# Kernel optimization log

Hardware: AMD Instinct MI355X
Metric: run time of the kernel (lower is better)

Reference implementation:

```python
import jax, jax.numpy as jnp
import numpy as np

B, L, D = 4, 2048, 2048
NH, HD, K = 32, 64, 16
LR = 1.0
EPS = 1e-6


def ln_fwd(x, gamma, beta):
    mu = x.mean(-1, keepdims=True)
    var = jnp.var(x, axis=-1, keepdims=True)
    x_hat = (x - mu) / jnp.sqrt(var + EPS)
    return gamma * x_hat + beta


def ln_fused_l2_bwd(x, target, gamma, beta):
    # grad of 0.5*||LN(x)-target||^2 wrt x (matches LayerNormFunction.backward
    # with grad_output = LN(x) - target)
    d = x.shape[-1]
    mu = x.mean(-1, keepdims=True)
    var = jnp.var(x, axis=-1, keepdims=True)
    std = jnp.sqrt(var + EPS)
    x_hat = (x - mu) / std
    y = gamma * x_hat + beta
    g = (y - target) * gamma
    return (d * g - g.sum(-1, keepdims=True) - x_hat * (g * x_hat).sum(-1, keepdims=True)) / (d * std)


def setup_inputs() -> dict:
    key = jax.random.key(0)
    ks = jax.random.split(key, 12)
    s = 0.02
    return {
        "hidden_states": jax.random.normal(ks[0], (B, L, D), jnp.float32),
        "Wq": jax.random.normal(ks[1], (D, D), jnp.float32) * s,
        "Wk": jax.random.normal(ks[2], (D, D), jnp.float32) * s,
        "Wv": jax.random.normal(ks[3], (D, D), jnp.float32) * s,
        "Wo": jax.random.normal(ks[4], (D, D), jnp.float32) * s,
        "linear_weight": jax.random.normal(ks[5], (NH, 1, D), jnp.float32) * s,
        "linear_bias": jnp.zeros((NH, 1), jnp.float32),
        "ln_weight": jnp.ones((NH, HD), jnp.float32),
        "ln_bias": jnp.zeros((NH, HD), jnp.float32),
        "W1_init": jax.random.normal(ks[6], (NH, HD, HD), jnp.float32) * s,
        "b1_init": jnp.zeros((NH, 1, HD), jnp.float32),
    }


def reference(hidden_states, Wq, Wk, Wv, Wo, linear_weight, linear_bias,
              ln_weight, ln_bias, W1_init, b1_init):
    Bq, Lq, Dq = hidden_states.shape
    n_chunk = Lq // K

    def split(x):  # [B,L,D] -> [B,NH,n_chunk,K,HD]
        return x.reshape(Bq, n_chunk, K, NH, HD).transpose(0, 3, 1, 2, 4)

    XC = split(hidden_states @ Wq.T)
    XB = split(hidden_states @ Wk.T)
    XA = split(hidden_states @ Wv.T)

    # inner-loop learning-rate coefficient: [B,NH,n_chunk,K,1]
    X = hidden_states.reshape(Bq, n_chunk, K, Dq)
    ilr = jnp.einsum('bnkd,hd->bhnk', X, linear_weight[:, 0, :]) + linear_bias[:, 0][None, :, None, None]
    ilr_gated = jax.nn.sigmoid(ilr)[..., None]
    token_idx = 1.0 / jnp.arange(1, K + 1, dtype=hidden_states.dtype)
    coeff = (LR * token_idx).reshape(1, 1, 1, K, 1) * ilr_gated / HD

    ln_w = ln_weight.reshape(1, NH, 1, HD)
    ln_b = ln_bias.reshape(1, NH, 1, HD)
    mask = jnp.tril(jnp.ones((K, K), hidden_states.dtype))

    W1 = jnp.broadcast_to(W1_init[None], (Bq, NH, HD, HD))
    b1 = jnp.broadcast_to(b1_init[None], (Bq, NH, 1, HD))

    def step(carry, inp):
        W1, b1 = carry
        xc, xb, xa, co = inp  # [B,NH,K,HD], co: [B,NH,K,1]
        Z1 = xb @ W1 + b1
        grad = ln_fused_l2_bwd(Z1, xa - xb, ln_w, ln_b)  # [B,NH,K,HD]
        Attn = mask * jnp.einsum('bhkf,bhjf->bhkj', xc, xb)
        E = mask * co.transpose(0, 1, 3, 2)  # E[i,j] = coeff_j * (j<=i)
        b1_bar = b1 - E @ grad
        Z1_bar = xc @ W1 - (Attn * E) @ grad + b1_bar
        W1_new = W1 - jnp.einsum('bhkf,bhkg->bhfg', co * xb, grad)
        b1_new = b1 - (co * grad).sum(-2, keepdims=True)
        out = xc + ln_fwd(Z1_bar, ln_w, ln_b)
        return (W1_new, b1_new), out

    xs = (XC.transpose(2, 0, 1, 3, 4), XB.transpose(2, 0, 1, 3, 4),
          XA.transpose(2, 0, 1, 3, 4), coeff.transpose(2, 0, 1, 3, 4))
    (_, _), outs = jax.lax.scan(step, (W1, b1), xs)
    # outs: [n_chunk,B,NH,K,HD] -> [B,L,D]
    XCW = outs.transpose(1, 0, 3, 2, 4).reshape(Bq, Lq, Dq)
    return XCW @ Wo.T
```

## Files before the change

kernel.cpp:

```cpp
#include <hip/hip_runtime.h>


typedef __attribute__((ext_vector_type(4))) float float4v;
typedef __attribute__((ext_vector_type(8))) __bf16 bf16x8;
typedef __attribute__((ext_vector_type(4))) short short4v;
typedef __attribute__((ext_vector_type(4))) unsigned int uint4v;

__device__ __forceinline__ unsigned short f2bf(float f) {
  unsigned int u = __builtin_bit_cast(unsigned int, f);
  u += 0x7FFFu + ((u >> 16) & 1u);
  return (unsigned short)(u >> 16);
}
__device__ __forceinline__ float bf2f(unsigned short s) {
  unsigned int u = ((unsigned int)s) << 16;
  return __builtin_bit_cast(float, u);
}
__device__ __forceinline__ void lds_load16(const void* g, void* l) {
  __builtin_amdgcn_global_load_lds((const __attribute__((address_space(1))) void*)g,
                                   (__attribute__((address_space(3))) void*)l, 16, 0, 0);
}

__device__ __forceinline__ void store_out(float* p, float v) { *p = v; }
__device__ __forceinline__ void store_out(unsigned short* p, float v) { *p = f2bf(v); }

template <typename OUT>
__global__ __launch_bounds__(256) void gemm_bt(
    const unsigned short* __restrict__ A, const unsigned short* __restrict__ B,
    OUT* __restrict__ C, int M, int N, int K) {
  __shared__ unsigned short sA[128 * 32];
  __shared__ unsigned short sB[128 * 32];
  const int tid = threadIdx.x;
  const int wave = tid >> 6;
  const int lane = tid & 63;
  const int quad = lane >> 4;
  const int l15 = lane & 15;
  const int wm = (wave >> 1) * 64;
  const int wn = (wave & 1) * 64;
  const int bm = blockIdx.y * 128;
  const int bn = blockIdx.x * 128;

  float4v acc[4][4];
#pragma unroll
  for (int i = 0; i < 4; ++i)
#pragma unroll
    for (int j = 0; j < 4; ++j) acc[i][j] = (float4v){0.f, 0.f, 0.f, 0.f};

  const int srow = tid >> 2;
  const int scol = (tid & 3) * 8;
  const unsigned short* aptr = A + (size_t)(bm + srow) * K + scol;
  const unsigned short* bptr = B + (size_t)(bn + srow) * K + scol;
  unsigned short* sAw0 = &sA[wave * 512];
  unsigned short* sAw1 = &sA[2048 + wave * 512];
  unsigned short* sBw0 = &sB[wave * 512];
  unsigned short* sBw1 = &sB[2048 + wave * 512];
  const size_t astep = (size_t)64 * K;

  for (int kt = 0; kt < K; kt += 32) {
    __syncthreads();
    lds_load16(aptr + kt, sAw0);
    lds_load16(aptr + kt + astep, sAw1);
    lds_load16(bptr + kt, sBw0);
    lds_load16(bptr + kt + astep, sBw1);
    __syncthreads();
    bf16x8 af[4], bf[4];
#pragma unroll
    for (int i = 0; i < 4; ++i)
      af[i] = *(const bf16x8*)&sA[(wm + i * 16 + l15) * 32 + quad * 8];
#pragma unroll
    for (int j = 0; j < 4; ++j)
      bf[j] = *(const bf16x8*)&sB[(wn + j * 16 + l15) * 32 + quad * 8];
#pragma unroll
    for (int i = 0; i < 4; ++i)
#pragma unroll
      for (int j = 0; j < 4; ++j)
        acc[i][j] = __builtin_amdgcn_mfma_f32_16x16x32_bf16(af[i], bf[j], acc[i][j], 0, 0, 0);
  }

#pragma unroll
  for (int i = 0; i < 4; ++i) {
    const int row0 = bm + wm + i * 16 + quad * 4;
#pragma unroll
    for (int j = 0; j < 4; ++j) {
      const int col = bn + wn + j * 16 + l15;
#pragma unroll
      for (int r = 0; r < 4; ++r)
        store_out(&C[(size_t)(row0 + r) * N + col], acc[i][j][r]);
    }
  }
}

__global__ __launch_bounds__(256) void f32_to_bf16_k(const float* __restrict__ s,
                                                     unsigned short* __restrict__ d, int n) {
  const int i = (blockIdx.x * 256 + threadIdx.x) * 8;
  if (i >= n) return;
  const float4v a = *(const float4v*)(s + i);
  const float4v b = *(const float4v*)(s + i + 4);
  uint4v o;
  o[0] = (unsigned int)f2bf(a[0]) | ((unsigned int)f2bf(a[1]) << 16);
  o[1] = (unsigned int)f2bf(a[2]) | ((unsigned int)f2bf(a[3]) << 16);
  o[2] = (unsigned int)f2bf(b[0]) | ((unsigned int)f2bf(b[1]) << 16);
  o[3] = (unsigned int)f2bf(b[2]) | ((unsigned int)f2bf(b[3]) << 16);
  *(uint4v*)(d + i) = o;
}

__global__ __launch_bounds__(256) void coeff_k(const unsigned short* __restrict__ ilr,
                                               const float* __restrict__ lb,
                                               float* __restrict__ coeff) {
  const int gid = blockIdx.x * 256 + threadIdx.x;
  const int row = gid >> 5;
  const int h = gid & 31;
  const float v = bf2f(ilr[row * 128 + h]) + lb[h];
  const float sig = 1.0f / (1.0f + __expf(-v));
  const int b = row >> 11;
  const int pos = row & 2047;
  const int cc = pos >> 4;
  const int k = pos & 15;
  coeff[((((size_t)b * 32 + h) * 128 + cc) << 4) + k] = sig / (64.0f * (float)(k + 1));
}

__global__ __launch_bounds__(64, 1) void ttt_scan(
    const unsigned short* __restrict__ XC, const unsigned short* __restrict__ XB,
    const unsigned short* __restrict__ XA, const float* __restrict__ coeff,
    const float* __restrict__ lnw, const float* __restrict__ lnb,
    const float* __restrict__ W1i, const float* __restrict__ b1i,
    unsigned short* __restrict__ XCW) {
  const int b = blockIdx.x >> 5;
  const int h = blockIdx.x & 31;
  const int lane = threadIdx.x;
  const int quad = lane >> 4;
  const int l15 = lane & 15;

  __shared__ float sW1T[64 * 68];
  __shared__ float sXCs[16 * 68];
  __shared__ float sXBs[16 * 68];
  __shared__ float sTs[16 * 68];
  __shared__ float sAttn[16 * 20];
  __shared__ float sB1[64];

  float gam[4], bet[4];
#pragma unroll
  for (int nt = 0; nt < 4; ++nt) {
    gam[nt] = lnw[h * 64 + nt * 16 + l15];
    bet[nt] = lnb[h * 64 + nt * 16 + l15];
  }
  float4v W1r[16];
#pragma unroll
  for (int mt = 0; mt < 4; ++mt)
#pragma unroll
    for (int nt = 0; nt < 4; ++nt) {
      float4v v;
#pragma unroll
      for (int r = 0; r < 4; ++r)
        v[r] = W1i[(size_t)h * 4096 + (size_t)(mt * 16 + quad * 4 + r) * 64 + nt * 16 + l15];
      W1r[mt * 4 + nt] = v;
    }
  sB1[lane] = b1i[h * 64 + lane];

  const int srow = lane >> 2;
  const int scol = (lane & 3) * 16;
  const size_t hdoff = (size_t)h * 64;
  const size_t browoff = (size_t)b * 2048;
  const size_t cobase = (((size_t)b * 32 + h) * 128) * 16;
  const float inv64 = 1.0f / 64.0f;
  const float4v zero4 = {0.f, 0.f, 0.f, 0.f};

  uint4v pxc0, pxc1, pxb0, pxb1, pxa0, pxa1;
  float pco;
  {
    const size_t goff = (browoff + (size_t)srow) * 2048 + hdoff + scol;
    pxc0 = *(const uint4v*)(XC + goff);
    pxc1 = *(const uint4v*)(XC + goff + 8);
    pxb0 = *(const uint4v*)(XB + goff);
    pxb1 = *(const uint4v*)(XB + goff + 8);
    pxa0 = *(const uint4v*)(XA + goff);
    pxa1 = *(const uint4v*)(XA + goff + 8);
    pco = coeff[cobase + l15];
  }

  for (int c = 0; c < 128; ++c) {
    const uint4v xc0 = pxc0, xc1 = pxc1, xb0 = pxb0, xb1 = pxb1, xa0 = pxa0, xa1 = pxa1;
    const float co = pco;
    {
      const int cn = (c < 127) ? c + 1 : 127;
      const size_t goff = (browoff + (size_t)(cn * 16 + srow)) * 2048 + hdoff + scol;
      pxc0 = *(const uint4v*)(XC + goff);
      pxc1 = *(const uint4v*)(XC + goff + 8);
      pxb0 = *(const uint4v*)(XB + goff);
      pxb1 = *(const uint4v*)(XB + goff + 8);
      pxa0 = *(const uint4v*)(XA + goff);
      pxa1 = *(const uint4v*)(XA + goff + 8);
      pco = coeff[cobase + (size_t)cn * 16 + l15];
    }

    float xcv[16], xbv[16], xav[16];
#pragma unroll
    for (int t2 = 0; t2 < 4; ++t2) {
      xcv[t2 * 2] = __builtin_bit_cast(float, xc0[t2] << 16);
      xcv[t2 * 2 + 1] = __builtin_bit_cast(float, xc0[t2] & 0xFFFF0000u);
      xcv[8 + t2 * 2] = __builtin_bit_cast(float, xc1[t2] << 16);
      xcv[8 + t2 * 2 + 1] = __builtin_bit_cast(float, xc1[t2] & 0xFFFF0000u);
      xbv[t2 * 2] = __builtin_bit_cast(float, xb0[t2] << 16);
      xbv[t2 * 2 + 1] = __builtin_bit_cast(float, xb0[t2] & 0xFFFF0000u);
      xbv[8 + t2 * 2] = __builtin_bit_cast(float, xb1[t2] << 16);
      xbv[8 + t2 * 2 + 1] = __builtin_bit_cast(float, xb1[t2] & 0xFFFF0000u);
      xav[t2 * 2] = __builtin_bit_cast(float, xa0[t2] << 16);
      xav[t2 * 2 + 1] = __builtin_bit_cast(float, xa0[t2] & 0xFFFF0000u);
      xav[8 + t2 * 2] = __builtin_bit_cast(float, xa1[t2] << 16);
      xav[8 + t2 * 2 + 1] = __builtin_bit_cast(float, xa1[t2] & 0xFFFF0000u);
    }
    const int sb = srow * 68 + scol;
#pragma unroll
    for (int e = 0; e < 16; ++e) {
      sXCs[sb + e] = xcv[e];
      sXBs[sb + e] = xbv[e];
      sTs[sb + e] = xav[e] - xbv[e];
    }
#pragma unroll
    for (int mt = 0; mt < 4; ++mt)
#pragma unroll
      for (int nt = 0; nt < 4; ++nt)
        *(float4v*)&sW1T[(nt * 16 + l15) * 68 + mt * 16 + quad * 4] = W1r[mt * 4 + nt];

    bf16x8 xbf[2], xcf[2];
#pragma unroll
    for (int hh = 0; hh < 2; ++hh) {
      const float4v pb0 = *(const float4v*)&sXBs[l15 * 68 + hh * 32 + quad * 8];
      const float4v pb1 = *(const float4v*)&sXBs[l15 * 68 + hh * 32 + quad * 8 + 4];
      const float4v pc0 = *(const float4v*)&sXCs[l15 * 68 + hh * 32 + quad * 8];
      const float4v pc1 = *(const float4v*)&sXCs[l15 * 68 + hh * 32 + quad * 8 + 4];
      bf16x8 fb, fc;
#pragma unroll
      for (int r = 0; r < 4; ++r) {
        fb[r] = (__bf16)pb0[r]; fb[4 + r] = (__bf16)pb1[r];
        fc[r] = (__bf16)pc0[r]; fc[4 + r] = (__bf16)pc1[r];
      }
      xbf[hh] = fb; xcf[hh] = fc;
    }
    bf16x8 w1f[4][2];
#pragma unroll
    for (int nt = 0; nt < 4; ++nt)
#pragma unroll
      for (int hh = 0; hh < 2; ++hh) {
        const float4v p0 = *(const float4v*)&sW1T[(nt * 16 + l15) * 68 + hh * 32 + quad * 8];
        const float4v p1 = *(const float4v*)&sW1T[(nt * 16 + l15) * 68 + hh * 32 + quad * 8 + 4];
        bf16x8 f;
#pragma unroll
        for (int r = 0; r < 4; ++r) { f[r] = (__bf16)p0[r]; f[4 + r] = (__bf16)p1[r]; }
        w1f[nt][hh] = f;
      }
    float cof[4];
#pragma unroll
    for (int r = 0; r < 4; ++r) cof[r] = __shfl(co, quad * 4 + r);
    float b1v[4];
#pragma unroll
    for (int nt = 0; nt < 4; ++nt) b1v[nt] = sB1[nt * 16 + l15];

    float4v z[4];
#pragma unroll
    for (int nt = 0; nt < 4; ++nt) {
      float4v t = __builtin_amdgcn_mfma_f32_16x16x32_bf16(xbf[0], w1f[nt][0], zero4, 0, 0, 0);
      t = __builtin_amdgcn_mfma_f32_16x16x32_bf16(xbf[1], w1f[nt][1], t, 0, 0, 0);
#pragma unroll
      for (int r = 0; r < 4; ++r) t[r] += b1v[nt];
      z[nt] = t;
    }

    float s1[4], s2[4];
#pragma unroll
    for (int r = 0; r < 4; ++r) {
      s1[r] = z[0][r] + z[1][r] + z[2][r] + z[3][r];
      s2[r] = z[0][r] * z[0][r] + z[1][r] * z[1][r] + z[2][r] * z[2][r] + z[3][r] * z[3][r];
    }
#pragma unroll
    for (int m = 1; m <= 8; m <<= 1)
#pragma unroll
      for (int r = 0; r < 4; ++r) {
        s1[r] += __shfl_xor(s1[r], m);
        s2[r] += __shfl_xor(s2[r], m);
      }
    float mu[4], rstd[4];
#pragma unroll
    for (int r = 0; r < 4; ++r) {
      mu[r] = s1[r] * inv64;
      const float var = s2[r] * inv64 - mu[r] * mu[r];
      rstd[r] = rsqrtf(var + 1e-6f);
    }
    float xh[4][4], gg[4][4];
#pragma unroll
    for (int nt = 0; nt < 4; ++nt)
#pragma unroll
      for (int r = 0; r < 4; ++r) {
        const float xhat = (z[nt][r] - mu[r]) * rstd[r];
        xh[nt][r] = xhat;
        const float y = gam[nt] * xhat + bet[nt];
        const float tgt = sTs[(quad * 4 + r) * 68 + nt * 16 + l15];
        gg[nt][r] = (y - tgt) * gam[nt];
      }
    float sg[4], sgx[4];
#pragma unroll
    for (int r = 0; r < 4; ++r) {
      sg[r] = gg[0][r] + gg[1][r] + gg[2][r] + gg[3][r];
      sgx[r] = gg[0][r] * xh[0][r] + gg[1][r] * xh[1][r] + gg[2][r] * xh[2][r] + gg[3][r] * xh[3][r];
    }
#pragma unroll
    for (int m = 1; m <= 8; m <<= 1)
#pragma unroll
      for (int r = 0; r < 4; ++r) {
        sg[r] += __shfl_xor(sg[r], m);
        sgx[r] += __shfl_xor(sgx[r], m);
      }
    float grad[4][4];
    short4v gradb[4];
#pragma unroll
    for (int nt = 0; nt < 4; ++nt)
#pragma unroll
      for (int r = 0; r < 4; ++r) {
        grad[nt][r] = (64.0f * gg[nt][r] - sg[r] - xh[nt][r] * sgx[r]) * (rstd[r] * inv64);
        gradb[nt][r] = (short)f2bf(grad[nt][r]);
      }

    float4v at = __builtin_amdgcn_mfma_f32_16x16x32_bf16(xcf[0], xbf[0], zero4, 0, 0, 0);
    at = __builtin_amdgcn_mfma_f32_16x16x32_bf16(xcf[1], xbf[1], at, 0, 0, 0);
#pragma unroll
    for (int r = 0; r < 4; ++r) sAttn[(quad * 4 + r) * 20 + l15] = at[r];
    const float4v av = *(const float4v*)&sAttn[l15 * 20 + quad * 4];
    short4v m1f;
#pragma unroll
    for (int jj = 0; jj < 4; ++jj) {
      const int k = quad * 4 + jj;
      const float e = (k <= l15) ? cof[jj] : 0.0f;
      m1f[jj] = (short)f2bf(-(av[jj] + 1.0f) * e);
    }

#pragma unroll
    for (int nt = 0; nt < 4; ++nt) {
      float4v t = __builtin_amdgcn_mfma_f32_16x16x32_bf16(xcf[0], w1f[nt][0], zero4, 0, 0, 0);
      t = __builtin_amdgcn_mfma_f32_16x16x32_bf16(xcf[1], w1f[nt][1], t, 0, 0, 0);
      t = __builtin_amdgcn_mfma_f32_16x16x16bf16_1k(m1f, gradb[nt], t, 0, 0, 0);
#pragma unroll
      for (int r = 0; r < 4; ++r) t[r] += b1v[nt];
      z[nt] = t;
    }

#pragma unroll
    for (int r = 0; r < 4; ++r) {
      s1[r] = z[0][r] + z[1][r] + z[2][r] + z[3][r];
      s2[r] = z[0][r] * z[0][r] + z[1][r] * z[1][r] + z[2][r] * z[2][r] + z[3][r] * z[3][r];
    }
#pragma unroll
    for (int m = 1; m <= 8; m <<= 1)
#pragma unroll
      for (int r = 0; r < 4; ++r) {
        s1[r] += __shfl_xor(s1[r], m);
        s2[r] += __shfl_xor(s2[r], m);
      }
#pragma unroll
    for (int r = 0; r < 4; ++r) {
      mu[r] = s1[r] * inv64;
      const float var = s2[r] * inv64 - mu[r] * mu[r];
      rstd[r] = rsqrtf(var + 1e-6f);
    }
#pragma unroll
    for (int nt = 0; nt < 4; ++nt)
#pragma unroll
      for (int r = 0; r < 4; ++r) {
        const float xhat = (z[nt][r] - mu[r]) * rstd[r];
        const float y = gam[nt] * xhat + bet[nt];
        const float o = sXCs[(quad * 4 + r) * 68 + nt * 16 + l15] + y;
        XCW[(browoff + (size_t)(c * 16 + quad * 4 + r)) * 2048 + hdoff + nt * 16 + l15] = f2bf(o);
      }

    float pb[4];
#pragma unroll
    for (int nt = 0; nt < 4; ++nt) {
      pb[nt] = cof[0] * grad[nt][0] + cof[1] * grad[nt][1] + cof[2] * grad[nt][2] + cof[3] * grad[nt][3];
      pb[nt] += __shfl_xor(pb[nt], 16);
      pb[nt] += __shfl_xor(pb[nt], 32);
    }
    if (lane < 16) {
#pragma unroll
      for (int nt = 0; nt < 4; ++nt) sB1[nt * 16 + lane] -= pb[nt];
    }

#pragma unroll
    for (int mt = 0; mt < 4; ++mt) {
      short4v caf;
#pragma unroll
      for (int jj = 0; jj < 4; ++jj)
        caf[jj] = (short)f2bf(-cof[jj] * sXBs[(quad * 4 + jj) * 68 + mt * 16 + l15]);
#pragma unroll
      for (int nt = 0; nt < 4; ++nt)
        W1r[mt * 4 + nt] =
            __builtin_amdgcn_mfma_f32_16x16x16bf16_1k(caf, gradb[nt], W1r[mt * 4 + nt], 0, 0, 0);
    }
  }
}

extern "C" void kernel_launch(void* const* d_in, const int* in_sizes, int n_in,
                              void* d_out, int out_size, void* d_ws, size_t ws_size,
                              hipStream_t stream) {
  const float* hs = (const float*)d_in[0];
  const float* Wq = (const float*)d_in[1];
  const float* Wk = (const float*)d_in[2];
  const float* Wv = (const float*)d_in[3];
  const float* Wo = (const float*)d_in[4];
  const float* lw = (const float*)d_in[5];
  const float* lb = (const float*)d_in[6];
  const float* lnw = (const float*)d_in[7];
  const float* lnb = (const float*)d_in[8];
  const float* W1i = (const float*)d_in[9];
  const float* b1i = (const float*)d_in[10];
  float* out = (float*)d_out;
  char* ws = (char*)d_ws;

  unsigned short* hsb = (unsigned short*)(ws);
  unsigned short* wqb = (unsigned short*)(ws + 33554432);
  unsigned short* wkb = (unsigned short*)(ws + 41943040);
  unsigned short* wvb = (unsigned short*)(ws + 50331648);
  unsigned short* wob = (unsigned short*)(ws + 58720256);
  unsigned short* lwb = (unsigned short*)(ws + 67108864);
  unsigned short* XCb = (unsigned short*)(ws + 67633152);
  unsigned short* XBb = (unsigned short*)(ws + 101187584);
  unsigned short* XAb = (unsigned short*)(ws + 134742016);
  unsigned short* ilrb = (unsigned short*)(ws + 168296448);
  float* coeff = (float*)(ws + 170393600);

  f32_to_bf16_k<<<8192, 256, 0, stream>>>(hs, hsb, 16777216);
  f32_to_bf16_k<<<2048, 256, 0, stream>>>(Wq, wqb, 4194304);
  f32_to_bf16_k<<<2048, 256, 0, stream>>>(Wk, wkb, 4194304);
  f32_to_bf16_k<<<2048, 256, 0, stream>>>(Wv, wvb, 4194304);
  f32_to_bf16_k<<<2048, 256, 0, stream>>>(Wo, wob, 4194304);
  hipMemsetAsync(lwb, 0, 524288, stream);
  f32_to_bf16_k<<<32, 256, 0, stream>>>(lw, lwb, 65536);

  dim3 blk(256);
  dim3 gbig(16, 64);
  gemm_bt<unsigned short><<<gbig, blk, 0, stream>>>(hsb, wqb, XCb, 8192, 2048, 2048);
  gemm_bt<unsigned short><<<gbig, blk, 0, stream>>>(hsb, wkb, XBb, 8192, 2048, 2048);
  gemm_bt<unsigned short><<<gbig, blk, 0, stream>>>(hsb, wvb, XAb, 8192, 2048, 2048);
  gemm_bt<unsigned short><<<dim3(1, 64), blk, 0, stream>>>(hsb, lwb, ilrb, 8192, 128, 2048);
  coeff_k<<<1024, 256, 0, stream>>>(ilrb, lb, coeff);
  ttt_scan<<<128, 64, 0, stream>>>(XCb, XBb, XAb, coeff, lnw, lnb, W1i, b1i, hsb);
  gemm_bt<float><<<gbig, blk, 0, stream>>>(hsb, wob, out, 8192, 2048, 2048);
}
```

Measured before the change: 1.050 ms.

## Keep W1 and inputs in MFMA register layout, drop per-chunk LDS transposes

The scan kernel no longer writes W1 to LDS transposed and re-reads it each chunk. It keeps a bf16-packed copy of W1 in registers that matches the 16x16x16 MFMA B-operand layout, so the ascending mt index can serve as the K dimension directly. XC and XB are now staged in LDS as raw bf16 and loaded as short4 fragments, with 16x16x16 MFMAs replacing 16x16x32 ones. The XC·W1 product is computed early so it is independent of the gradient. b1 now lives in registers, and a cheaper perm-based bf16 packing replaces the old conversion. This shortens the serial per-chunk critical path at the cost of more registers and twice as many MFMA issues per product.

```diff
diff --git a/kernel.cpp b/kernel.cpp
--- a/kernel.cpp
+++ b/kernel.cpp
@@ -2,9 +2,10 @@
 
 
 typedef __attribute__((ext_vector_type(4))) float float4v;
+typedef __attribute__((ext_vector_type(4))) short short4v;
+typedef __attribute__((ext_vector_type(2))) unsigned int uint2v;
+typedef __attribute__((ext_vector_type(4))) unsigned int uint4v;
 typedef __attribute__((ext_vector_type(8))) __bf16 bf16x8;
-typedef __attribute__((ext_vector_type(4))) short short4v;
-typedef __attribute__((ext_vector_type(4))) unsigned int uint4v;
 
 __device__ __forceinline__ unsigned short f2bf(float f) {
   unsigned int u = __builtin_bit_cast(unsigned int, f);
@@ -14,6 +15,17 @@
 __device__ __forceinline__ float bf2f(unsigned short s) {
   unsigned int u = ((unsigned int)s) << 16;
   return __builtin_bit_cast(float, u);
+}
+__device__ __forceinline__ unsigned int pkbf(float a, float b) {
+  const unsigned int ua = __builtin_bit_cast(unsigned int, a) + 0x8000u;
+  const unsigned int ub = __builtin_bit_cast(unsigned int, b) + 0x8000u;
+  return __builtin_amdgcn_perm(ub, ua, 0x07060302u);
+}
+__device__ __forceinline__ short4v pkbf4(float4v v) {
+  uint2v u;
+  u[0] = pkbf(v[0], v[1]);
+  u[1] = pkbf(v[2], v[3]);
+  return __builtin_bit_cast(short4v, u);
 }
 __device__ __forceinline__ void lds_load16(const void* g, void* l) {
   __builtin_amdgcn_global_load_lds((const __attribute__((address_space(1))) void*)g,
@@ -130,20 +142,20 @@
   const int quad = lane >> 4;
   const int l15 = lane & 15;
 
-  __shared__ float sW1T[64 * 68];
-  __shared__ float sXCs[16 * 68];
-  __shared__ float sXBs[16 * 68];
+  __shared__ unsigned short sXCr[16 * 64];
+  __shared__ unsigned short sXBr[16 * 64];
   __shared__ float sTs[16 * 68];
   __shared__ float sAttn[16 * 20];
-  __shared__ float sB1[64];
-
-  float gam[4], bet[4];
+
+  float gam[4], bet[4], b1v[4];
 #pragma unroll
   for (int nt = 0; nt < 4; ++nt) {
     gam[nt] = lnw[h * 64 + nt * 16 + l15];
     bet[nt] = lnb[h * 64 + nt * 16 + l15];
+    b1v[nt] = b1i[h * 64 + nt * 16 + l15];
   }
   float4v W1r[16];
+  short4v w1b[16];
 #pragma unroll
   for (int mt = 0; mt < 4; ++mt)
 #pragma unroll
@@ -153,8 +165,8 @@
       for (int r = 0; r < 4; ++r)
         v[r] = W1i[(size_t)h * 4096 + (size_t)(mt * 16 + quad * 4 + r) * 64 + nt * 16 + l15];
       W1r[mt * 4 + nt] = v;
-    }
-  sB1[lane] = b1i[h * 64 + lane];
+      w1b[mt * 4 + nt] = pkbf4(v);
+    }
 
   const int srow = lane >> 2;
   const int scol = (lane & 3) * 16;
@@ -192,77 +204,81 @@
       pco = coeff[cobase + (size_t)cn * 16 + l15];
     }
 
-    float xcv[16], xbv[16], xav[16];
-#pragma unroll
-    for (int t2 = 0; t2 < 4; ++t2) {
-      xcv[t2 * 2] = __builtin_bit_cast(float, xc0[t2] << 16);
-      xcv[t2 * 2 + 1] = __builtin_bit_cast(float, xc0[t2] & 0xFFFF0000u);
-      xcv[8 + t2 * 2] = __builtin_bit_cast(float, xc1[t2] << 16);
-      xcv[8 + t2 * 2 + 1] = __builtin_bit_cast(float, xc1[t2] & 0xFFFF0000u);
-      xbv[t2 * 2] = __builtin_bit_cast(float, xb0[t2] << 16);
-      xbv[t2 * 2 + 1] = __builtin_bit_cast(float, xb0[t2] & 0xFFFF0000u);
-      xbv[8 + t2 * 2] = __builtin_bit_cast(float, xb1[t2] << 16);
-      xbv[8 + t2 * 2 + 1] = __builtin_bit_cast(float, xb1[t2] & 0xFFFF0000u);
-      xav[t2 * 2] = __builtin_bit_cast(float, xa0[t2] << 16);
-      xav[t2 * 2 + 1] = __builtin_bit_cast(float, xa0[t2] & 0xFFFF0000u);
-      xav[8 + t2 * 2] = __builtin_bit_cast(float, xa1[t2] << 16);
-      xav[8 + t2 * 2 + 1] = __builtin_bit_cast(float, xa1[t2] & 0xFFFF0000u);
-    }
-    const int sb = srow * 68 + scol;
-#pragma unroll
-    for (int e = 0; e < 16; ++e) {
-      sXCs[sb + e] = xcv[e];
-      sXBs[sb + e] = xbv[e];
-      sTs[sb + e] = xav[e] - xbv[e];
-    }
-#pragma unroll
-    for (int mt = 0; mt < 4; ++mt)
-#pragma unroll
-      for (int nt = 0; nt < 4; ++nt)
-        *(float4v*)&sW1T[(nt * 16 + l15) * 68 + mt * 16 + quad * 4] = W1r[mt * 4 + nt];
-
-    bf16x8 xbf[2], xcf[2];
-#pragma unroll
-    for (int hh = 0; hh < 2; ++hh) {
-      const float4v pb0 = *(const float4v*)&sXBs[l15 * 68 + hh * 32 + quad * 8];
-      const float4v pb1 = *(const float4v*)&sXBs[l15 * 68 + hh * 32 + quad * 8 + 4];
-      const float4v pc0 = *(const float4v*)&sXCs[l15 * 68 + hh * 32 + quad * 8];
-      const float4v pc1 = *(const float4v*)&sXCs[l15 * 68 + hh * 32 + quad * 8 + 4];
-      bf16x8 fb, fc;
-#pragma unroll
-      for (int r = 0; r < 4; ++r) {
-        fb[r] = (__bf16)pb0[r]; fb[4 + r] = (__bf16)pb1[r];
-        fc[r] = (__bf16)pc0[r]; fc[4 + r] = (__bf16)pc1[r];
-      }
-      xbf[hh] = fb; xcf[hh] = fc;
-    }
-    bf16x8 w1f[4][2];
-#pragma unroll
-    for (int nt = 0; nt < 4; ++nt)
-#pragma unroll
-      for (int hh = 0; hh < 2; ++hh) {
-        const float4v p0 = *(const float4v*)&sW1T[(nt * 16 + l15) * 68 + hh * 32 + quad * 8];
-        const float4v p1 = *(const float4v*)&sW1T[(nt * 16 + l15) * 68 + hh * 32 + quad * 8 + 4];
-        bf16x8 f;
-#pragma unroll
-        for (int r = 0; r < 4; ++r) { f[r] = (__bf16)p0[r]; f[4 + r] = (__bf16)p1[r]; }
-        w1f[nt][hh] = f;
-      }
+    *(uint4v*)&sXCr[srow * 64 + scol] = xc0;
+    *(uint4v*)&sXCr[srow * 64 + scol + 8] = xc1;
+    *(uint4v*)&sXBr[srow * 64 + scol] = xb0;
+    *(uint4v*)&sXBr[srow * 64 + scol + 8] = xb1;
+    {
+      float tv[16];
+#pragma unroll
+      for (int t2 = 0; t2 < 4; ++t2) {
+        const float blo = __builtin_bit_cast(float, xb0[t2] << 16);
+        const float bhi = __builtin_bit_cast(float, xb0[t2] & 0xFFFF0000u);
+        const float alo = __builtin_bit_cast(float, xa0[t2] << 16);
+        const float ahi = __builtin_bit_cast(float, xa0[t2] & 0xFFFF0000u);
+        tv[t2 * 2] = alo - blo;
+        tv[t2 * 2 + 1] = ahi - bhi;
+        const float blo1 = __builtin_bit_cast(float, xb1[t2] << 16);
+        const float bhi1 = __builtin_bit_cast(float, xb1[t2] & 0xFFFF0000u);
+        const float alo1 = __builtin_bit_cast(float, xa1[t2] << 16);
+        const float ahi1 = __builtin_bit_cast(float, xa1[t2] & 0xFFFF0000u);
+        tv[8 + t2 * 2] = alo1 - blo1;
+        tv[8 + t2 * 2 + 1] = ahi1 - bhi1;
+      }
+#pragma unroll
+      for (int k4 = 0; k4 < 4; ++k4)
+        *(float4v*)&sTs[srow * 68 + scol + k4 * 4] =
+            (float4v){tv[k4 * 4], tv[k4 * 4 + 1], tv[k4 * 4 + 2], tv[k4 * 4 + 3]};
+    }
+
+    short4v xbA[4], xcA[4];
+#pragma unroll
+    for (int mt = 0; mt < 4; ++mt) {
+      xbA[mt] = *(const short4v*)&sXBr[l15 * 64 + mt * 16 + quad * 4];
+      xcA[mt] = *(const short4v*)&sXCr[l15 * 64 + mt * 16 + quad * 4];
+    }
     float cof[4];
 #pragma unroll
     for (int r = 0; r < 4; ++r) cof[r] = __shfl(co, quad * 4 + r);
-    float b1v[4];
-#pragma unroll
-    for (int nt = 0; nt < 4; ++nt) b1v[nt] = sB1[nt * 16 + l15];
+
+    short4v caf[4];
+#pragma unroll
+    for (int mt = 0; mt < 4; ++mt) {
+      float4v cv;
+#pragma unroll
+      for (int jj = 0; jj < 4; ++jj) {
+        const unsigned int raw = sXBr[(quad * 4 + jj) * 64 + mt * 16 + l15];
+        cv[jj] = -cof[jj] * __builtin_bit_cast(float, raw << 16);
+      }
+      caf[mt] = pkbf4(cv);
+    }
+
+    float4v at = __builtin_amdgcn_mfma_f32_16x16x16bf16_1k(xcA[0], xbA[0], zero4, 0, 0, 0);
+    at = __builtin_amdgcn_mfma_f32_16x16x16bf16_1k(xcA[1], xbA[1], at, 0, 0, 0);
+    at = __builtin_amdgcn_mfma_f32_16x16x16bf16_1k(xcA[2], xbA[2], at, 0, 0, 0);
+    at = __builtin_amdgcn_mfma_f32_16x16x16bf16_1k(xcA[3], xbA[3], at, 0, 0, 0);
+#pragma unroll
+    for (int r = 0; r < 4; ++r) sAttn[(quad * 4 + r) * 20 + l15] = at[r];
 
     float4v z[4];
 #pragma unroll
     for (int nt = 0; nt < 4; ++nt) {
-      float4v t = __builtin_amdgcn_mfma_f32_16x16x32_bf16(xbf[0], w1f[nt][0], zero4, 0, 0, 0);
-      t = __builtin_amdgcn_mfma_f32_16x16x32_bf16(xbf[1], w1f[nt][1], t, 0, 0, 0);
+      float4v t = __builtin_amdgcn_mfma_f32_16x16x16bf16_1k(xbA[0], w1b[nt], zero4, 0, 0, 0);
+      t = __builtin_amdgcn_mfma_f32_16x16x16bf16_1k(xbA[1], w1b[4 + nt], t, 0, 0, 0);
+      t = __builtin_amdgcn_mfma_f32_16x16x16bf16_1k(xbA[2], w1b[8 + nt], t, 0, 0, 0);
+      t = __builtin_amdgcn_mfma_f32_16x16x16bf16_1k(xbA[3], w1b[12 + nt], t, 0, 0, 0);
 #pragma unroll
       for (int r = 0; r < 4; ++r) t[r] += b1v[nt];
       z[nt] = t;
+    }
+    float4v zb[4];
+#pragma unroll
+    for (int nt = 0; nt < 4; ++nt) {
+      float4v t = __builtin_amdgcn_mfma_f32_16x16x16bf16_1k(xcA[0], w1b[nt], zero4, 0, 0, 0);
+      t = __builtin_amdgcn_mfma_f32_16x16x16bf16_1k(xcA[1], w1b[4 + nt], t, 0, 0, 0);
+      t = __builtin_amdgcn_mfma_f32_16x16x16bf16_1k(xcA[2], w1b[8 + nt], t, 0, 0, 0);
+      t = __builtin_amdgcn_mfma_f32_16x16x16bf16_1k(xcA[3], w1b[12 + nt], t, 0, 0, 0);
+      zb[nt] = t;
     }
 
     float s1[4], s2[4];
@@ -312,31 +328,32 @@
     float grad[4][4];
     short4v gradb[4];
 #pragma unroll
-    for (int nt = 0; nt < 4; ++nt)
-#pragma unroll
-      for (int r = 0; r < 4; ++r) {
-        grad[nt][r] = (64.0f * gg[nt][r] - sg[r] - xh[nt][r] * sgx[r]) * (rstd[r] * inv64);
-        gradb[nt][r] = (short)f2bf(grad[nt][r]);
-      }
-
-    float4v at = __builtin_amdgcn_mfma_f32_16x16x32_bf16(xcf[0], xbf[0], zero4, 0, 0, 0);
-    at = __builtin_amdgcn_mfma_f32_16x16x32_bf16(xcf[1], xbf[1], at, 0, 0, 0);
-#pragma unroll
-    for (int r = 0; r < 4; ++r) sAttn[(quad * 4 + r) * 20 + l15] = at[r];
+    for (int nt = 0; nt < 4; ++nt) {
+      float4v gv;
+#pragma unroll
+      for (int r = 0; r < 4; ++r) {
+        gv[r] = (64.0f * gg[nt][r] - sg[r] - xh[nt][r] * sgx[r]) * (rstd[r] * inv64);
+        grad[nt][r] = gv[r];
+      }
+      gradb[nt] = pkbf4(gv);
+    }
+
     const float4v av = *(const float4v*)&sAttn[l15 * 20 + quad * 4];
     short4v m1f;
-#pragma unroll
-    for (int jj = 0; jj < 4; ++jj) {
-      const int k = quad * 4 + jj;
-      const float e = (k <= l15) ? cof[jj] : 0.0f;
-      m1f[jj] = (short)f2bf(-(av[jj] + 1.0f) * e);
-    }
-
-#pragma unroll
-    for (int nt = 0; nt < 4; ++nt) {
-      float4v t = __builtin_amdgcn_mfma_f32_16x16x32_bf16(xcf[0], w1f[nt][0], zero4, 0, 0, 0);
-      t = __builtin_amdgcn_mfma_f32_16x16x32_bf16(xcf[1], w1f[nt][1], t, 0, 0, 0);
-      t = __builtin_amdgcn_mfma_f32_16x16x16bf16_1k(m1f, gradb[nt], t, 0, 0, 0);
+    {
+      float4v mv;
+#pragma unroll
+      for (int jj = 0; jj < 4; ++jj) {
+        const int k = quad * 4 + jj;
+        const float e = (k <= l15) ? cof[jj] : 0.0f;
+        mv[jj] = -(av[jj] + 1.0f) * e;
+      }
+      m1f = pkbf4(mv);
+    }
+
+#pragma unroll
+    for (int nt = 0; nt < 4; ++nt) {
+      float4v t = __builtin_amdgcn_mfma_f32_16x16x16bf16_1k(m1f, gradb[nt], zb[nt], 0, 0, 0);
 #pragma unroll
       for (int r = 0; r < 4; ++r) t[r] += b1v[nt];
       z[nt] = t;
@@ -366,33 +383,28 @@
       for (int r = 0; r < 4; ++r) {
         const float xhat = (z[nt][r] - mu[r]) * rstd[r];
         const float y = gam[nt] * xhat + bet[nt];
-        const float o = sXCs[(quad * 4 + r) * 68 + nt * 16 + l15] + y;
-        XCW[(browoff + (size_t)(c * 16 + quad * 4 + r)) * 2048 + hdoff + nt * 16 + l15] = f2bf(o);
-      }
-
-    float pb[4];
-#pragma unroll
-    for (int nt = 0; nt < 4; ++nt) {
-      pb[nt] = cof[0] * grad[nt][0] + cof[1] * grad[nt][1] + cof[2] * grad[nt][2] + cof[3] * grad[nt][3];
-      pb[nt] += __shfl_xor(pb[nt], 16);
-      pb[nt] += __shfl_xor(pb[nt], 32);
-    }
-    if (lane < 16) {
-#pragma unroll
-      for (int nt = 0; nt < 4; ++nt) sB1[nt * 16 + lane] -= pb[nt];
-    }
-
-#pragma unroll
-    for (int mt = 0; mt < 4; ++mt) {
-      short4v caf;
-#pragma unroll
-      for (int jj = 0; jj < 4; ++jj)
-        caf[jj] = (short)f2bf(-cof[jj] * sXBs[(quad * 4 + jj) * 68 + mt * 16 + l15]);
-#pragma unroll
-      for (int nt = 0; nt < 4; ++nt)
+        const float xcv = bf2f(sXCr[(quad * 4 + r) * 64 + nt * 16 + l15]);
+        XCW[(browoff + (size_t)(c * 16 + quad * 4 + r)) * 2048 + hdoff + nt * 16 + l15] =
+            f2bf(xcv + y);
+      }
+
+#pragma unroll
+    for (int nt = 0; nt < 4; ++nt) {
+      float pb = cof[0] * grad[nt][0] + cof[1] * grad[nt][1] + cof[2] * grad[nt][2] +
+                 cof[3] * grad[nt][3];
+      pb += __shfl_xor(pb, 16);
+      pb += __shfl_xor(pb, 32);
+      b1v[nt] -= pb;
+    }
+
+#pragma unroll
+    for (int mt = 0; mt < 4; ++mt)
+#pragma unroll
+      for (int nt = 0; nt < 4; ++nt) {
         W1r[mt * 4 + nt] =
-            __builtin_amdgcn_mfma_f32_16x16x16bf16_1k(caf, gradb[nt], W1r[mt * 4 + nt], 0, 0, 0);
-    }
+            __builtin_amdgcn_mfma_f32_16x16x16bf16_1k(caf[mt], gradb[nt], W1r[mt * 4 + nt], 0, 0, 0);
+        w1b[mt * 4 + nt] = pkbf4(W1r[mt * 4 + nt]);
+      }
   }
 }
 
```

Result: slower. 1.139 ms (+8.5%).
